# Kernel optimization log

Hardware: AMD Instinct MI355X
Metric: run time of the kernel (lower is better)

Reference implementation:

```python
import jax, jax.numpy as jnp
import numpy as np
import math

N_EMBD = 1024
N_HEAD = 16
N_LAYER = 12


def setup_inputs() -> dict:
    key = jax.random.key(0)
    kx, kw, kb = jax.random.split(key, 3)
    B, T, C = 4, 2048, N_EMBD
    x = jax.random.normal(kx, (B, T, C), dtype=jnp.float32)
    # nn.Linear(C, 3C): weight [3C, C] scaled by 1/sqrt(2*n_layer), bias [3C]
    bound = 1.0 / math.sqrt(C)
    W = jax.random.uniform(kw, (3 * C, C), minval=-bound, maxval=bound, dtype=jnp.float32)
    W = W * (1.0 / math.sqrt(N_LAYER * 2))
    b = jax.random.uniform(kb, (3 * C,), minval=-bound, maxval=bound, dtype=jnp.float32)
    return {"x": x, "W": W, "b": b}


def reference(x, W, b) -> jnp.ndarray:
    B, T, C = x.shape
    H = N_HEAD
    D = C // H
    qkv = jnp.einsum("btc,oc->bto", x, W) + b  # [B, T, 3C]
    q, k, v = jnp.split(qkv, 3, axis=-1)
    # [B, H, T, D]
    q = q.reshape(B, T, H, D).transpose(0, 2, 1, 3)
    k = k.reshape(B, T, H, D).transpose(0, 2, 1, 3)
    v = v.reshape(B, T, H, D).transpose(0, 2, 1, 3)
    att = jnp.einsum("bhtd,bhsd->bhts", q, k) / math.sqrt(D)  # [B, H, T, T]
    causal = jnp.tril(jnp.ones((T, T), dtype=bool))
    att = jnp.where(causal, att, -jnp.inf)
    att = jax.nn.softmax(att, axis=-1)
    y = jnp.einsum("bhts,bhsd->bhtd", att, v)  # [B, H, T, D]
    return y.transpose(0, 2, 1, 3).reshape(B, T, C)
```

## Files before the change

### kernel.cpp

```cpp
#include <hip/hip_runtime.h>


typedef __attribute__((ext_vector_type(8))) short short8;
typedef __attribute__((ext_vector_type(4))) short s16x4;
typedef __attribute__((ext_vector_type(4))) float f32x4;

#define AS1 __attribute__((address_space(1)))
#define AS3 __attribute__((address_space(3)))

__device__ __forceinline__ unsigned short f2bf(float f) {
  unsigned int u = __float_as_uint(f);
  u += 0x7fffu + ((u >> 16) & 1u);
  return (unsigned short)(u >> 16);
}

__device__ __forceinline__ unsigned int pack_bf16(float lo, float hi) {
  return __builtin_amdgcn_perm(__float_as_uint(hi) + 0x8000u,
                               __float_as_uint(lo) + 0x8000u, 0x07060302u);
}

__device__ __forceinline__ void async_copy16(const unsigned short* g, unsigned short* l) {
  const AS1 unsigned char* gp = (const AS1 unsigned char*)(unsigned long long)(uintptr_t)g;
  AS3 unsigned char* lp = (AS3 unsigned char*)(unsigned int)(uintptr_t)l;
  __builtin_amdgcn_global_load_lds((const AS1 void*)gp, (AS3 void*)lp, 16, 0, 0);
}

__global__ __launch_bounds__(256) void cvt_both(const float* __restrict__ x,
                                                const float* __restrict__ W,
                                                unsigned short* __restrict__ xt,
                                                unsigned short* __restrict__ wt) {
  int i = blockIdx.x * 256 + threadIdx.x;
  const float* in;
  unsigned short* out;
  int k;
  if (i < 1048576) { in = x; out = xt; k = i; }
  else             { in = W; out = wt; k = i - 1048576; }
  int row = k >> 7, colg = k & 127;
  int bt = row >> 7, r7 = row & 127;
  int frag = (r7 >> 6) * 8 + ((r7 >> 4) & 3) * 2 + ((colg >> 2) & 1);
  int kt = colg >> 3;
  int dst = ((bt * 16 + kt) * 16 + frag) * 512 + ((colg & 3) * 16 + (row & 15)) * 8;
  const float4* p = (const float4*)in + (size_t)k * 2;
  float4 a = p[0], b = p[1];
  uint4 o;
  o.x = (unsigned)f2bf(a.x) | ((unsigned)f2bf(a.y) << 16);
  o.y = (unsigned)f2bf(a.z) | ((unsigned)f2bf(a.w) << 16);
  o.z = (unsigned)f2bf(b.x) | ((unsigned)f2bf(b.y) << 16);
  o.w = (unsigned)f2bf(b.z) | ((unsigned)f2bf(b.w) << 16);
  *(uint4*)(out + dst) = o;
}

__global__ __launch_bounds__(256) void qkv_gemm(const unsigned short* __restrict__ xt,
                                                const unsigned short* __restrict__ wt,
                                                const float* __restrict__ bias,
                                                unsigned short* __restrict__ qb,
                                                unsigned short* __restrict__ kvb) {
  __shared__ unsigned short As[2][8192];
  __shared__ unsigned short Bs[2][8192];
  int tid = threadIdx.x;
  int wave = tid >> 6, lane = tid & 63;
  int q4 = lane >> 4, l16 = lane & 15;
  int bm = blockIdx.x, bn = blockIdx.y;

  f32x4 zero = {0.f, 0.f, 0.f, 0.f};
  f32x4 acc[4][4];
#pragma unroll
  for (int i = 0; i < 4; ++i)
#pragma unroll
    for (int j = 0; j < 4; ++j) acc[i][j] = zero;

  const unsigned short* Abase = xt + (size_t)bm * 16 * 8192;
  const unsigned short* Bbase = wt + (size_t)bn * 16 * 8192;

  auto stageAB = [&](int d, int kt) {
    const unsigned short* ga = Abase + (size_t)kt * 8192;
    const unsigned short* gb = Bbase + (size_t)kt * 8192;
#pragma unroll
    for (int i2 = 0; i2 < 4; ++i2) {
      int u = i2 * 256 + wave * 64;
      async_copy16(ga + (u + lane) * 8, &As[d][u * 8]);
      async_copy16(gb + (u + lane) * 8, &Bs[d][u * 8]);
    }
  };

  stageAB(0, 0);
  for (int kt = 0; kt < 16; ++kt) {
    __syncthreads();
    if (kt < 15) stageAB((kt + 1) & 1, kt + 1);
    const unsigned short* Ac = As[kt & 1];
    const unsigned short* Bc = Bs[kt & 1];
#pragma unroll
    for (int ks = 0; ks < 2; ++ks) {
      short8 af[4], bf[4];
#pragma unroll
      for (int i = 0; i < 4; ++i)
        af[i] = *(const short8*)(Ac + ((wave & 1) * 8 + i * 2 + ks) * 512 + lane * 8);
#pragma unroll
      for (int j = 0; j < 4; ++j)
        bf[j] = *(const short8*)(Bc + ((wave >> 1) * 8 + j * 2 + ks) * 512 + lane * 8);
#pragma unroll
      for (int i = 0; i < 4; ++i)
#pragma unroll
        for (int j = 0; j < 4; ++j)
          acc[i][j] = __builtin_amdgcn_mfma_f32_16x16x32_bf16(af[i], bf[j], acc[i][j], 0, 0, 0);
    }
  }

  const float QSCALE = 0.18033688011112042f;
  int rowbase = bm * 128 + (wave & 1) * 64;
  int colbase = bn * 128 + (wave >> 1) * 64;
#pragma unroll
  for (int j = 0; j < 4; ++j) {
    int o = colbase + j * 16 + l16;
    float bv = bias[o];
#pragma unroll
    for (int i = 0; i < 4; ++i) {
      int r0 = rowbase + i * 16 + q4 * 4;
      int b = r0 >> 11, t0 = r0 & 2047;
      if (o < 1024) {
        int h = o >> 6, d = o & 63;
#pragma unroll
        for (int r = 0; r < 4; ++r)
          qb[((((size_t)b * 16 + h) * 2048 + t0 + r) << 6) + d] =
              f2bf((acc[i][j][r] + bv) * QSCALE);
      } else if (o < 2048) {
        int o2 = o - 1024;
        int h = o2 >> 6, dd = o2 & 63;
        int st = t0 >> 6, s6 = t0 & 63;
        int ns = s6 >> 4, l16p = s6 & 15;
        int ks = dd >> 5, q4p = (dd & 31) >> 3, jj = dd & 7;
        size_t base = ((size_t)(b * 16 + h) * 32 + st) * 8192 +
                      ((ns * 2 + ks) * 64 + q4p * 16 + l16p) * 8 + jj;
#pragma unroll
        for (int r = 0; r < 4; ++r)
          kvb[base + r * 8] = f2bf(acc[i][j][r] + bv);
      } else {
        int o3 = o - 2048;
        int h = o3 >> 6, dd = o3 & 63;
        int st = t0 >> 6, s6 = t0 & 63;
        int ns = s6 >> 4, q4p = (s6 >> 2) & 3;
        int p = dd >> 5, halfd = (dd >> 4) & 1, l16p = dd & 15;
        size_t base = ((size_t)(b * 16 + h) * 32 + st) * 8192 + 4096 +
                      ((ns * 2 + p) * 64 + q4p * 16 + l16p) * 8 + halfd * 4;
        ushort4 pk;
        pk.x = f2bf(acc[i][j][0] + bv);
        pk.y = f2bf(acc[i][j][1] + bv);
        pk.z = f2bf(acc[i][j][2] + bv);
        pk.w = f2bf(acc[i][j][3] + bv);
        *(ushort4*)(&kvb[base]) = pk;
      }
    }
  }
}

__global__ __launch_bounds__(128, 4) void flash_attn(const unsigned short* __restrict__ qb,
                                                     const unsigned short* __restrict__ kvb,
                                                     float* __restrict__ out) {
  __shared__ unsigned short buf[2][8192];

  const int tid = threadIdx.x;
  const int wave = tid >> 6, lane = tid & 63;
  const int q4 = lane >> 4, l16 = lane & 15;
  const int n = blockIdx.x;
  const int bh = (n & 7) * 8 + ((n >> 3) & 7);
  const int bx = n >> 6;
  const int b = bh >> 4, h = bh & 15;

  const unsigned short* Qg = qb + (size_t)bh * (2048 * 64);
  const unsigned short* KVg = kvb + (size_t)bh * 32 * 8192;
  const s16x4 ones = {(short)0x3F80, (short)0x3F80, (short)0x3F80, (short)0x3F80};

  auto stage = [&](int d, int st) {
    const unsigned short* tp = KVg + (size_t)st * 8192;
#pragma unroll
    for (int i2 = 0; i2 < 8; ++i2) {
      int u = i2 * 128 + wave * 64;
      async_copy16(tp + (u + lane) * 8, &buf[d][u * 8]);
    }
  };

  for (int pass = 0; pass < 2; ++pass) {
    const int qt = pass ? 31 - bx : bx;
    const int t0w = qt * 64 + wave * 32;

    short8 qf[2][2];
#pragma unroll
    for (int mt = 0; mt < 2; ++mt)
#pragma unroll
      for (int ks = 0; ks < 2; ++ks)
        qf[mt][ks] = *(const short8*)(Qg + (size_t)(t0w + mt * 16 + l16) * 64 +
                                      ks * 32 + q4 * 8);

    f32x4 zero = {0.f, 0.f, 0.f, 0.f};
    f32x4 oT[2][4];
#pragma unroll
    for (int mt = 0; mt < 2; ++mt)
#pragma unroll
      for (int nd = 0; nd < 4; ++nd) oT[mt][nd] = zero;
    f32x4 l_acc[2] = {zero, zero};

    __syncthreads();
    stage(0, 0);
    for (int st = 0; st <= qt; ++st) {
      __syncthreads();
      if (st < qt) stage((st + 1) & 1, st + 1);
      const unsigned short* cur = buf[st & 1];

      f32x4 sT[2][4];
#pragma unroll
      for (int ns = 0; ns < 4; ++ns) {
        short8 kf0 = *(const short8*)(cur + (ns * 2 + 0) * 512 + lane * 8);
        short8 kf1 = *(const short8*)(cur + (ns * 2 + 1) * 512 + lane * 8);
#pragma unroll
        for (int mt = 0; mt < 2; ++mt) {
          sT[mt][ns] = __builtin_amdgcn_mfma_f32_16x16x32_bf16(kf0, qf[mt][0], zero, 0, 0, 0);
          sT[mt][ns] = __builtin_amdgcn_mfma_f32_16x16x32_bf16(kf1, qf[mt][1], sT[mt][ns], 0, 0, 0);
        }
      }

      if (st == qt) {
#pragma unroll
        for (int mt = 0; mt < 2; ++mt) {
          int tg = t0w + mt * 16 + l16;
#pragma unroll
          for (int ns = 0; ns < 4; ++ns) {
            int sgb = st * 64 + ns * 16 + q4 * 4;
#pragma unroll
            for (int r = 0; r < 4; ++r)
              if (sgb + r > tg) sT[mt][ns][r] = -3.0e38f;
          }
        }
      }

#pragma unroll
      for (int ns = 0; ns < 4; ++ns) {
        s16x4 pf[2];
#pragma unroll
        for (int mt = 0; mt < 2; ++mt) {
          union { unsigned int u[2]; s16x4 s4; } pu;
          pu.u[0] = pack_bf16(__builtin_amdgcn_exp2f(sT[mt][ns][0]),
                              __builtin_amdgcn_exp2f(sT[mt][ns][1]));
          pu.u[1] = pack_bf16(__builtin_amdgcn_exp2f(sT[mt][ns][2]),
                              __builtin_amdgcn_exp2f(sT[mt][ns][3]));
          pf[mt] = pu.s4;
        }
#pragma unroll
        for (int p = 0; p < 2; ++p) {
          short8 v8 = *(const short8*)(cur + 4096 + ((ns * 2 + p) * 64 + lane) * 8);
          s16x4 vlo = __builtin_shufflevector(v8, v8, 0, 1, 2, 3);
          s16x4 vhi = __builtin_shufflevector(v8, v8, 4, 5, 6, 7);
#pragma unroll
          for (int mt = 0; mt < 2; ++mt) {
            oT[mt][2 * p] = __builtin_amdgcn_mfma_f32_16x16x16bf16_1k(vlo, pf[mt], oT[mt][2 * p], 0, 0, 0);
            oT[mt][2 * p + 1] = __builtin_amdgcn_mfma_f32_16x16x16bf16_1k(vhi, pf[mt], oT[mt][2 * p + 1], 0, 0, 0);
          }
        }
#pragma unroll
        for (int mt = 0; mt < 2; ++mt)
          l_acc[mt] = __builtin_amdgcn_mfma_f32_16x16x16bf16_1k(ones, pf[mt], l_acc[mt], 0, 0, 0);
      }
    }

#pragma unroll
    for (int mt = 0; mt < 2; ++mt) {
      float inv = 1.0f / l_acc[mt][0];
      int t = t0w + mt * 16 + l16;
      float* op = out + (size_t)(b * 2048 + t) * 1024 + h * 64 + q4 * 4;
#pragma unroll
      for (int nd = 0; nd < 4; ++nd) {
        float4 o4 = {oT[mt][nd][0] * inv, oT[mt][nd][1] * inv,
                     oT[mt][nd][2] * inv, oT[mt][nd][3] * inv};
        *(float4*)(op + nd * 16) = o4;
      }
    }
  }
}

extern "C" void kernel_launch(void* const* d_in, const int* in_sizes, int n_in,
                              void* d_out, int out_size, void* d_ws, size_t ws_size,
                              hipStream_t stream) {
  const float* x = (const float*)d_in[0];
  const float* W = (const float*)d_in[1];
  const float* bias = (const float*)d_in[2];
  float* out = (float*)d_out;

  char* ws = (char*)d_ws;
  unsigned short* xt = (unsigned short*)(ws);
  unsigned short* wt = (unsigned short*)(ws + 16777216);
  unsigned short* qb = (unsigned short*)(ws + 23068672);
  unsigned short* kvb = (unsigned short*)(ws + 39845888);

  hipLaunchKernelGGL(cvt_both, dim3(5632), dim3(256), 0, stream, x, W, xt, wt);
  hipLaunchKernelGGL(qkv_gemm, dim3(64, 24), dim3(256), 0, stream, xt, wt, bias,
                     qb, kvb);
  hipLaunchKernelGGL(flash_attn, dim3(1024), dim3(128), 0, stream, qb, kvb, out);
}
```

Baseline: 211.6 us.

## Halve GEMM K-tile to 32 and make convert kernel write-coalesced

The QKV GEMM now stages K-slices of 32 instead of 64, halving the LDS buffers and running 32 pipeline steps instead of 16, which could raise occupancy at the cost of more barriers. The conversion kernel now iterates over output positions so bf16 stores are contiguous, while the fp32 reads become strided gathers. It also swaps the round-to-nearest-even conversion for a cheaper perm-based round-half-up pack.

```diff
diff --git a/kernel.cpp b/kernel.cpp
--- a/kernel.cpp
+++ b/kernel.cpp
@@ -29,25 +29,23 @@
                                                 const float* __restrict__ W,
                                                 unsigned short* __restrict__ xt,
                                                 unsigned short* __restrict__ wt) {
-  int i = blockIdx.x * 256 + threadIdx.x;
+  int U = blockIdx.x * 256 + threadIdx.x;
   const float* in;
   unsigned short* out;
-  int k;
-  if (i < 1048576) { in = x; out = xt; k = i; }
-  else             { in = W; out = wt; k = i - 1048576; }
-  int row = k >> 7, colg = k & 127;
-  int bt = row >> 7, r7 = row & 127;
-  int frag = (r7 >> 6) * 8 + ((r7 >> 4) & 3) * 2 + ((colg >> 2) & 1);
-  int kt = colg >> 3;
-  int dst = ((bt * 16 + kt) * 16 + frag) * 512 + ((colg & 3) * 16 + (row & 15)) * 8;
-  const float4* p = (const float4*)in + (size_t)k * 2;
+  if (U < 1048576) { in = x; out = xt; }
+  else             { in = W; out = wt; U -= 1048576; }
+  int u6 = U & 63, frag = (U >> 6) & 15, kt = (U >> 10) & 15, bt = U >> 14;
+  int ks = frag & 1, i = (frag >> 1) & 3, half = frag >> 3;
+  int row = bt * 128 + half * 64 + i * 16 + (u6 & 15);
+  int colf = kt * 64 + ks * 32 + (u6 >> 4) * 8;
+  const float4* p = (const float4*)(in + (size_t)row * 1024 + colf);
   float4 a = p[0], b = p[1];
   uint4 o;
-  o.x = (unsigned)f2bf(a.x) | ((unsigned)f2bf(a.y) << 16);
-  o.y = (unsigned)f2bf(a.z) | ((unsigned)f2bf(a.w) << 16);
-  o.z = (unsigned)f2bf(b.x) | ((unsigned)f2bf(b.y) << 16);
-  o.w = (unsigned)f2bf(b.z) | ((unsigned)f2bf(b.w) << 16);
-  *(uint4*)(out + dst) = o;
+  o.x = pack_bf16(a.x, a.y);
+  o.y = pack_bf16(a.z, a.w);
+  o.z = pack_bf16(b.x, b.y);
+  o.w = pack_bf16(b.z, b.w);
+  *(uint4*)(out + (size_t)U * 8) = o;
 }
 
 __global__ __launch_bounds__(256) void qkv_gemm(const unsigned short* __restrict__ xt,
@@ -55,8 +53,8 @@
                                                 const float* __restrict__ bias,
                                                 unsigned short* __restrict__ qb,
                                                 unsigned short* __restrict__ kvb) {
-  __shared__ unsigned short As[2][8192];
-  __shared__ unsigned short Bs[2][8192];
+  __shared__ unsigned short As[2][4096];
+  __shared__ unsigned short Bs[2][4096];
   int tid = threadIdx.x;
   int wave = tid >> 6, lane = tid & 63;
   int q4 = lane >> 4, l16 = lane & 15;
@@ -72,38 +70,37 @@
   const unsigned short* Abase = xt + (size_t)bm * 16 * 8192;
   const unsigned short* Bbase = wt + (size_t)bn * 16 * 8192;
 
-  auto stageAB = [&](int d, int kt) {
-    const unsigned short* ga = Abase + (size_t)kt * 8192;
-    const unsigned short* gb = Bbase + (size_t)kt * 8192;
-#pragma unroll
-    for (int i2 = 0; i2 < 4; ++i2) {
-      int u = i2 * 256 + wave * 64;
-      async_copy16(ga + (u + lane) * 8, &As[d][u * 8]);
-      async_copy16(gb + (u + lane) * 8, &Bs[d][u * 8]);
+  auto stage = [&](int d, int kt32) {
+    int kt64 = kt32 >> 1, ks = kt32 & 1;
+    const unsigned short* ga = Abase + (size_t)kt64 * 8192;
+    const unsigned short* gb = Bbase + (size_t)kt64 * 8192;
+#pragma unroll
+    for (int j = 0; j < 2; ++j) {
+      int fi = wave * 2 + j;
+      int f = (fi >> 2) * 8 + (fi & 3) * 2 + ks;
+      async_copy16(ga + f * 512 + lane * 8, &As[d][fi * 512]);
+      async_copy16(gb + f * 512 + lane * 8, &Bs[d][fi * 512]);
     }
   };
 
-  stageAB(0, 0);
-  for (int kt = 0; kt < 16; ++kt) {
+  stage(0, 0);
+  for (int kt = 0; kt < 32; ++kt) {
     __syncthreads();
-    if (kt < 15) stageAB((kt + 1) & 1, kt + 1);
+    if (kt < 31) stage((kt + 1) & 1, kt + 1);
     const unsigned short* Ac = As[kt & 1];
     const unsigned short* Bc = Bs[kt & 1];
-#pragma unroll
-    for (int ks = 0; ks < 2; ++ks) {
-      short8 af[4], bf[4];
-#pragma unroll
-      for (int i = 0; i < 4; ++i)
-        af[i] = *(const short8*)(Ac + ((wave & 1) * 8 + i * 2 + ks) * 512 + lane * 8);
+    short8 af[4], bf[4];
+#pragma unroll
+    for (int i = 0; i < 4; ++i)
+      af[i] = *(const short8*)(Ac + ((wave & 1) * 4 + i) * 512 + lane * 8);
+#pragma unroll
+    for (int j = 0; j < 4; ++j)
+      bf[j] = *(const short8*)(Bc + ((wave >> 1) * 4 + j) * 512 + lane * 8);
+#pragma unroll
+    for (int i = 0; i < 4; ++i)
 #pragma unroll
       for (int j = 0; j < 4; ++j)
-        bf[j] = *(const short8*)(Bc + ((wave >> 1) * 8 + j * 2 + ks) * 512 + lane * 8);
-#pragma unroll
-      for (int i = 0; i < 4; ++i)
-#pragma unroll
-        for (int j = 0; j < 4; ++j)
-          acc[i][j] = __builtin_amdgcn_mfma_f32_16x16x32_bf16(af[i], bf[j], acc[i][j], 0, 0, 0);
-    }
+        acc[i][j] = __builtin_amdgcn_mfma_f32_16x16x32_bf16(af[i], bf[j], acc[i][j], 0, 0, 0);
   }
 
   const float QSCALE = 0.18033688011112042f;
```

Result: faster. 204.2 us (-3.5%).
